# Kernel tuning notes

Measured on AMD Instinct MI355X. Metric: run time of the kernel, lower is better.

The kernel has to match this reference:

```python
import jax, jax.numpy as jnp
import numpy as np
import math

D = 1024
H = 16
DH = D // H
FF = 4096
B, S = 2, 2048


def _layernorm(x, g, b, eps=1e-5):
    mu = jnp.mean(x, axis=-1, keepdims=True)
    var = jnp.var(x, axis=-1, keepdims=True)
    return (x - mu) * jax.lax.rsqrt(var + eps) * g + b


def _gelu_tanh(x):
    # 0.5*x*(1+tanh(sqrt(2/pi)*(x+0.044715*x^3)))
    c = math.sqrt(2.0 / math.pi)
    return 0.5 * x * (1.0 + jnp.tanh(c * (x + 0.044715 * x ** 3)))


def setup_inputs() -> dict:
    key = jax.random.key(0)
    ks = jax.random.split(key, 8)
    s = 0.02
    return {
        "x": jax.random.normal(ks[0], (B, S, D), dtype=jnp.float32),
        "ln1_g": jnp.ones((D,), jnp.float32),
        "ln1_b": jnp.zeros((D,), jnp.float32),
        "Wqkv": jax.random.normal(ks[1], (D, 3 * D), jnp.float32) * s,
        "bqkv": jnp.zeros((3 * D,), jnp.float32),
        "Wo": jax.random.normal(ks[2], (D, D), jnp.float32) * s,
        "bo": jnp.zeros((D,), jnp.float32),
        "ln2_g": jnp.ones((D,), jnp.float32),
        "ln2_b": jnp.zeros((D,), jnp.float32),
        "W1": jax.random.normal(ks[3], (D, FF), jnp.float32) * s,
        "b1": jnp.zeros((FF,), jnp.float32),
        "W2": jax.random.normal(ks[4], (FF, D), jnp.float32) * s,
        "b2": jnp.zeros((D,), jnp.float32),
    }


def reference(x, ln1_g, ln1_b, Wqkv, bqkv, Wo, bo, ln2_g, ln2_b, W1, b1, W2, b2):
    b, s, d = x.shape
    h = _layernorm(x, ln1_g, ln1_b)
    qkv = h @ Wqkv + bqkv                       # [B,S,3D]
    q, k, v = jnp.split(qkv, 3, axis=-1)
    q = q.reshape(b, s, H, DH).transpose(0, 2, 1, 3)   # [B,H,S,Dh]
    k = k.reshape(b, s, H, DH).transpose(0, 2, 1, 3)
    v = v.reshape(b, s, H, DH).transpose(0, 2, 1, 3)
    scores = jnp.einsum("bhqd,bhkd->bhqk", q, k) / math.sqrt(DH)
    probs = jax.nn.softmax(scores, axis=-1)
    attn = jnp.einsum("bhqk,bhkd->bhqd", probs, v)     # [B,H,S,Dh]
    attn = attn.transpose(0, 2, 1, 3).reshape(b, s, d)
    attn = attn @ Wo + bo
    x = x + attn
    m = _layernorm(x, ln2_g, ln2_b)
    m = _gelu_tanh(m @ W1 + b1) @ W2 + b2
    return x + m
```

## Files before the change

### kernel.cpp

```cpp
#include <hip/hip_runtime.h>
#include <hip/hip_bf16.h>
#include <cstdint>

#define D_ 1024
#define H_ 16
#define DH_ 64
#define FF_ 4096
#define B_ 2
#define S_ 2048
#define MR_ (B_ * S_)

typedef __bf16 bf16x8 __attribute__((ext_vector_type(8)));
typedef __bf16 bf16x4 __attribute__((ext_vector_type(4)));
typedef float f32x4 __attribute__((ext_vector_type(4)));
typedef float f32x16 __attribute__((ext_vector_type(16)));

__device__ __forceinline__ void g2lds16(const void* g, void* l) {
  __builtin_amdgcn_global_load_lds(
      (__attribute__((address_space(1))) void*)(uintptr_t)g,
      (__attribute__((address_space(3))) void*)(uint32_t)(uintptr_t)l,
      16, 0, 0);
}

__device__ __forceinline__ unsigned pkbf16(float lo, float hi) {
  unsigned r;
  asm("v_cvt_pk_bf16_f32 %0, %1, %2" : "=v"(r) : "v"(lo), "v"(hi));
  return r;
}

__device__ __forceinline__ float fexp2(float x) {
  return __builtin_amdgcn_exp2f(x);
}

__global__ __launch_bounds__(256) void transpose_all(
    const float* __restrict__ W0, __hip_bfloat16* __restrict__ T0,
    const float* __restrict__ W1p, __hip_bfloat16* __restrict__ T1,
    const float* __restrict__ W2p, __hip_bfloat16* __restrict__ T2,
    const float* __restrict__ W3p, __hip_bfloat16* __restrict__ T3) {
  __shared__ float t[32][33];
  int ti = blockIdx.x;
  const float* W;
  __hip_bfloat16* Wt;
  int K, N, loc;
  if (ti < 3072)      { W = W0;  Wt = T0; K = 1024; N = 3072; loc = ti; }
  else if (ti < 4096) { W = W1p; Wt = T1; K = 1024; N = 1024; loc = ti - 3072; }
  else if (ti < 8192) { W = W2p; Wt = T2; K = 1024; N = 4096; loc = ti - 4096; }
  else                { W = W3p; Wt = T3; K = 4096; N = 1024; loc = ti - 8192; }
  int ntn = N >> 5;
  int bx = (loc % ntn) * 32;
  int by = (loc / ntn) * 32;
  int tx = threadIdx.x & 31, ty = threadIdx.x >> 5;
#pragma unroll
  for (int i = 0; i < 4; ++i)
    t[ty + 8 * i][tx] = W[(size_t)(by + ty + 8 * i) * N + bx + tx];
  __syncthreads();
#pragma unroll
  for (int i = 0; i < 4; ++i)
    Wt[(size_t)(bx + ty + 8 * i) * K + by + tx] = __float2bfloat16(t[tx][ty + 8 * i]);
}

__global__ __launch_bounds__(256) void ln_kernel(
    const float* __restrict__ x, const float* __restrict__ g,
    const float* __restrict__ b, __hip_bfloat16* __restrict__ out) {
  int row = blockIdx.x;
  const float4* xr = (const float4*)(x + (size_t)row * D_);
  float4 v = xr[threadIdx.x];
  float s = v.x + v.y + v.z + v.w;
  float ss = v.x * v.x + v.y * v.y + v.z * v.z + v.w * v.w;
#pragma unroll
  for (int m = 1; m < 64; m <<= 1) {
    s += __shfl_xor(s, m);
    ss += __shfl_xor(ss, m);
  }
  __shared__ float rs[4], rss[4];
  int wave = threadIdx.x >> 6, lane = threadIdx.x & 63;
  if (lane == 0) { rs[wave] = s; rss[wave] = ss; }
  __syncthreads();
  s = rs[0] + rs[1] + rs[2] + rs[3];
  ss = rss[0] + rss[1] + rss[2] + rss[3];
  float mean = s * (1.0f / D_);
  float var = ss * (1.0f / D_) - mean * mean;
  float inv = rsqrtf(var + 1e-5f);
  int c = threadIdx.x * 4;
  float4 gv = ((const float4*)g)[threadIdx.x];
  float4 bv = ((const float4*)b)[threadIdx.x];
  __hip_bfloat16* o = out + (size_t)row * D_ + c;
  o[0] = __float2bfloat16((v.x - mean) * inv * gv.x + bv.x);
  o[1] = __float2bfloat16((v.y - mean) * inv * gv.y + bv.y);
  o[2] = __float2bfloat16((v.z - mean) * inv * gv.z + bv.z);
  o[3] = __float2bfloat16((v.w - mean) * inv * gv.w + bv.w);
}

template <int EPI>
__global__ __launch_bounds__(256) void gemm4(
    const __hip_bfloat16* __restrict__ A, const __hip_bfloat16* __restrict__ Bt,
    const float* __restrict__ bias, const float* __restrict__ resid,
    void* __restrict__ outp, __hip_bfloat16* __restrict__ vt, int M, int N, int K) {
  constexpr int BM = 128, BN = 128, MF = 4, NF = 4;
  __shared__ alignas(16) __hip_bfloat16 sA[2][BM * 64];
  __shared__ alignas(16) __hip_bfloat16 sB[2][BN * 64];
  const int tid = threadIdx.x;
  const int lane = tid & 63, wave = tid >> 6;
  const int l15 = lane & 15, l4 = lane >> 4;
  const int wr = wave >> 1, wc = wave & 1;
  const int csw = (l15 & 7) << 3;

  const int gx = gridDim.x;
  int nwg = gx * gridDim.y;
  int flat = blockIdx.y * gx + blockIdx.x;
  int cpx = nwg >> 3;
  int swz = (flat & 7) * cpx + (flat >> 3);
  const int m0 = (swz / gx) * BM, n0 = (swz % gx) * BN;

  f32x4 z = {0.f, 0.f, 0.f, 0.f};
  f32x4 acc[MF][NF];
#pragma unroll
  for (int i = 0; i < MF; ++i)
#pragma unroll
    for (int j = 0; j < NF; ++j) acc[i][j] = z;

  auto stage = [&](int bu, int kt) {
#pragma unroll
    for (int it = 0; it < 4; ++it) {
      int idx = it * 256 + tid;
      int r = idx >> 3, c = (idx & 7) * 8;
      int cs = c ^ ((r & 7) << 3);
      g2lds16(A + (size_t)(m0 + r) * K + kt + cs, (void*)(&sA[bu][idx * 8]));
      g2lds16(Bt + (size_t)(n0 + r) * K + kt + cs, (void*)(&sB[bu][idx * 8]));
    }
  };

  const int nk = K / 64;
  stage(0, 0);
  asm volatile("s_waitcnt vmcnt(0)" ::: "memory");
  __builtin_amdgcn_s_barrier();

  for (int j = 0; j < nk; ++j) {
    const int cur = j & 1;
    if (j + 1 < nk) stage(cur ^ 1, (j + 1) * 64);

    __builtin_amdgcn_s_setprio(1);
#pragma unroll
    for (int kk = 0; kk < 2; ++kk) {
      int col = (kk * 32 + l4 * 8) ^ csw;
      bf16x8 bfr[NF];
#pragma unroll
      for (int nf = 0; nf < NF; ++nf)
        bfr[nf] = *(const bf16x8*)(&sB[cur][(wc * 64 + nf * 16 + l15) * 64 + col]);
#pragma unroll
      for (int mf = 0; mf < MF; ++mf) {
        bf16x8 af = *(const bf16x8*)(&sA[cur][(wr * 64 + mf * 16 + l15) * 64 + col]);
#pragma unroll
        for (int nf = 0; nf < NF; ++nf)
          acc[mf][nf] =
              __builtin_amdgcn_mfma_f32_16x16x32_bf16(af, bfr[nf], acc[mf][nf], 0, 0, 0);
      }
    }
    __builtin_amdgcn_s_setprio(0);

    asm volatile("s_waitcnt lgkmcnt(0)" ::: "memory");
    __builtin_amdgcn_sched_barrier(0);
    asm volatile("s_waitcnt vmcnt(0)" ::: "memory");
    __builtin_amdgcn_s_barrier();
    asm volatile("" ::: "memory");
  }

#pragma unroll
  for (int mf = 0; mf < MF; ++mf) {
#pragma unroll
    for (int nf = 0; nf < NF; ++nf) {
      int col = n0 + wc * 64 + nf * 16 + l15;
      float bv = bias[col];
      if (EPI == 3 && col >= 2 * D_) {
        int d = col - 2 * D_;
        int srow0 = m0 + wr * 64 + mf * 16 + l4 * 4;
        int bb = srow0 >> 11, s0 = srow0 & (S_ - 1);
        bf16x4 ov;
#pragma unroll
        for (int j = 0; j < 4; ++j) ov[j] = (__bf16)(acc[mf][nf][j] + bv);
        *(bf16x4*)(vt + ((size_t)(bb * H_ + (d >> 6)) * DH_ + (d & 63)) * S_ + s0) = ov;
      } else {
#pragma unroll
        for (int j = 0; j < 4; ++j) {
          int row = m0 + wr * 64 + mf * 16 + l4 * 4 + j;
          size_t o = (size_t)row * N + col;
          float v = acc[mf][nf][j] + bv;
          if (EPI == 0 || EPI == 3) {
            ((__hip_bfloat16*)outp)[o] = __float2bfloat16(v);
          } else if (EPI == 1) {
            ((float*)outp)[o] = v + resid[o];
          } else {
            float a = 0.7978845608028654f * (v + 0.044715f * v * v * v);
            a = fminf(fmaxf(a, -15.f), 15.f);
            float e = __expf(2.f * a);
            float th = (e - 1.f) / (e + 1.f);
            ((__hip_bfloat16*)outp)[o] = __float2bfloat16(0.5f * v * (1.f + th));
          }
        }
      }
    }
  }
}

template <int EPI>
__global__ __launch_bounds__(256) void gemm64r3(
    const __hip_bfloat16* __restrict__ A, const __hip_bfloat16* __restrict__ Bt,
    const float* __restrict__ bias, const float* __restrict__ resid,
    void* __restrict__ outp, int M, int N, int K) {
  constexpr int BM = 128, BN = 64, MF = 4, NF = 2;
  __shared__ alignas(16) __hip_bfloat16 sA[3][BM * 64];
  __shared__ alignas(16) __hip_bfloat16 sB[3][BN * 64];
  const int tid = threadIdx.x;
  const int lane = tid & 63, wave = tid >> 6;
  const int l15 = lane & 15, l4 = lane >> 4;
  const int wr = wave >> 1, wc = wave & 1;
  const int csw = (l15 & 7) << 3;

  const int gx = gridDim.x;
  int nwg = gx * gridDim.y;
  int flat = blockIdx.y * gx + blockIdx.x;
  int cpx = nwg >> 3;
  int swz = (flat & 7) * cpx + (flat >> 3);
  const int m0 = (swz / gx) * BM, n0 = (swz % gx) * BN;

  f32x4 z = {0.f, 0.f, 0.f, 0.f};
  f32x4 acc[MF][NF];
#pragma unroll
  for (int i = 0; i < MF; ++i)
#pragma unroll
    for (int j = 0; j < NF; ++j) acc[i][j] = z;

  auto stage = [&](int bu, int kt) {
#pragma unroll
    for (int it = 0; it < 4; ++it) {
      int idx = it * 256 + tid;
      int r = idx >> 3, c = (idx & 7) * 8;
      int cs = c ^ ((r & 7) << 3);
      g2lds16(A + (size_t)(m0 + r) * K + kt + cs, (void*)(&sA[bu][idx * 8]));
    }
#pragma unroll
    for (int it = 0; it < 2; ++it) {
      int idx = it * 256 + tid;
      int r = idx >> 3, c = (idx & 7) * 8;
      int cs = c ^ ((r & 7) << 3);
      g2lds16(Bt + (size_t)(n0 + r) * K + kt + cs, (void*)(&sB[bu][idx * 8]));
    }
  };

  const int nk = K / 64;
  stage(0, 0);
  stage(1, 64);
  asm volatile("s_waitcnt vmcnt(6)" ::: "memory");
  __builtin_amdgcn_s_barrier();

  int bu = 0, bu2 = 2;
  for (int j = 0; j < nk; ++j) {
    const bool pf = (j + 2) < nk;
    if (pf) stage(bu2, (j + 2) * 64);

    __builtin_amdgcn_s_setprio(1);
#pragma unroll
    for (int kk = 0; kk < 2; ++kk) {
      int col = (kk * 32 + l4 * 8) ^ csw;
      bf16x8 bfr[NF];
#pragma unroll
      for (int nf = 0; nf < NF; ++nf)
        bfr[nf] = *(const bf16x8*)(&sB[bu][(wc * 32 + nf * 16 + l15) * 64 + col]);
#pragma unroll
      for (int mf = 0; mf < MF; ++mf) {
        bf16x8 af = *(const bf16x8*)(&sA[bu][(wr * 64 + mf * 16 + l15) * 64 + col]);
#pragma unroll
        for (int nf = 0; nf < NF; ++nf)
          acc[mf][nf] =
              __builtin_amdgcn_mfma_f32_16x16x32_bf16(af, bfr[nf], acc[mf][nf], 0, 0, 0);
      }
    }
    __builtin_amdgcn_s_setprio(0);

    asm volatile("s_waitcnt lgkmcnt(0)" ::: "memory");
    __builtin_amdgcn_sched_barrier(0);
    if (pf)
      asm volatile("s_waitcnt vmcnt(6)" ::: "memory");
    else
      asm volatile("s_waitcnt vmcnt(0)" ::: "memory");
    __builtin_amdgcn_s_barrier();
    asm volatile("" ::: "memory");
    bu = (bu == 2) ? 0 : bu + 1;
    bu2 = (bu2 == 2) ? 0 : bu2 + 1;
  }

#pragma unroll
  for (int mf = 0; mf < MF; ++mf) {
#pragma unroll
    for (int nf = 0; nf < NF; ++nf) {
      int col = n0 + wc * 32 + nf * 16 + l15;
      float bv = bias[col];
#pragma unroll
      for (int j = 0; j < 4; ++j) {
        int row = m0 + wr * 64 + mf * 16 + l4 * 4 + j;
        size_t o = (size_t)row * N + col;
        float v = acc[mf][nf][j] + bv;
        if (EPI == 0) {
          ((__hip_bfloat16*)outp)[o] = __float2bfloat16(v);
        } else if (EPI == 1) {
          ((float*)outp)[o] = v + resid[o];
        } else {
          float a = 0.7978845608028654f * (v + 0.044715f * v * v * v);
          a = fminf(fmaxf(a, -15.f), 15.f);
          float e = __expf(2.f * a);
          float th = (e - 1.f) / (e + 1.f);
          ((__hip_bfloat16*)outp)[o] = __float2bfloat16(0.5f * v * (1.f + th));
        }
      }
    }
  }
}

template <int EPI>
__global__ __launch_bounds__(512, 1) void gemm256(
    const __hip_bfloat16* __restrict__ A, const __hip_bfloat16* __restrict__ Bt,
    const float* __restrict__ bias, const float* __restrict__ resid,
    void* __restrict__ outp, int M, int N, int K) {
  constexpr int BM = 256, BN = 256, MF = 8, NF = 4, WN = 4;
  __shared__ alignas(16) __hip_bfloat16 sA[2][BM * 64];
  __shared__ alignas(16) __hip_bfloat16 sB[2][BN * 64];
  const int tid = threadIdx.x;
  const int lane = tid & 63, wave = tid >> 6;
  const int l15 = lane & 15, l4 = lane >> 4;
  const int wr = wave / WN, wc = wave % WN;
  const int csw = (l15 & 7) << 3;

  const int gx = gridDim.x;
  int nwg = gx * gridDim.y;
  int flat = blockIdx.y * gx + blockIdx.x;
  int cpx = nwg >> 3;
  int swz = (flat & 7) * cpx + (flat >> 3);
  const int m0 = (swz / gx) * BM, n0 = (swz % gx) * BN;

  f32x4 z = {0.f, 0.f, 0.f, 0.f};
  f32x4 acc[MF][NF];
#pragma unroll
  for (int i = 0; i < MF; ++i)
#pragma unroll
    for (int j = 0; j < NF; ++j) acc[i][j] = z;

  auto stage = [&](int bu, int kt) {
#pragma unroll
    for (int it = 0; it < 4; ++it) {
      int idx = it * 512 + tid;
      int r = idx >> 3, c = (idx & 7) * 8;
      int cs = c ^ ((r & 7) << 3);
      g2lds16(A + (size_t)(m0 + r) * K + kt + cs, (void*)(&sA[bu][idx * 8]));
      g2lds16(Bt + (size_t)(n0 + r) * K + kt + cs, (void*)(&sB[bu][idx * 8]));
    }
  };

  const int nk = K / 64;
  stage(0, 0);
  asm volatile("s_waitcnt vmcnt(0)" ::: "memory");
  __builtin_amdgcn_s_barrier();

  for (int j = 0; j < nk; ++j) {
    const int cur = j & 1;
    if (j + 1 < nk) stage(cur ^ 1, (j + 1) * 64);

    __builtin_amdgcn_s_setprio(1);
#pragma unroll
    for (int kk = 0; kk < 2; ++kk) {
      int col = (kk * 32 + l4 * 8) ^ csw;
      bf16x8 bfr[NF];
#pragma unroll
      for (int nf = 0; nf < NF; ++nf)
        bfr[nf] = *(const bf16x8*)(&sB[cur][(wc * 64 + nf * 16 + l15) * 64 + col]);
#pragma unroll
      for (int mf = 0; mf < MF; ++mf) {
        bf16x8 af = *(const bf16x8*)(&sA[cur][(wr * 128 + mf * 16 + l15) * 64 + col]);
#pragma unroll
        for (int nf = 0; nf < NF; ++nf)
          acc[mf][nf] =
              __builtin_amdgcn_mfma_f32_16x16x32_bf16(af, bfr[nf], acc[mf][nf], 0, 0, 0);
      }
    }
    __builtin_amdgcn_s_setprio(0);

    asm volatile("s_waitcnt lgkmcnt(0)" ::: "memory");
    __builtin_amdgcn_sched_barrier(0);
    asm volatile("s_waitcnt vmcnt(0)" ::: "memory");
    __builtin_amdgcn_s_barrier();
    asm volatile("" ::: "memory");
  }

#pragma unroll
  for (int mf = 0; mf < MF; ++mf) {
#pragma unroll
    for (int nf = 0; nf < NF; ++nf) {
      int col = n0 + wc * 64 + nf * 16 + l15;
      float bv = bias[col];
#pragma unroll
      for (int j = 0; j < 4; ++j) {
        int row = m0 + wr * 128 + mf * 16 + l4 * 4 + j;
        size_t o = (size_t)row * N + col;
        float v = acc[mf][nf][j] + bv;
        if (EPI == 0) {
          ((__hip_bfloat16*)outp)[o] = __float2bfloat16(v);
        } else if (EPI == 1) {
          ((float*)outp)[o] = v + resid[o];
        } else {
          float a = 0.7978845608028654f * (v + 0.044715f * v * v * v);
          a = fminf(fmaxf(a, -15.f), 15.f);
          float e = __expf(2.f * a);
          float th = (e - 1.f) / (e + 1.f);
          ((__hip_bfloat16*)outp)[o] = __float2bfloat16(0.5f * v * (1.f + th));
        }
      }
    }
  }
}

__global__ __launch_bounds__(256, 2) void attn_kernel(
    const __hip_bfloat16* __restrict__ qkv, const __hip_bfloat16* __restrict__ vT,
    __hip_bfloat16* __restrict__ out) {
  __shared__ alignas(16) __hip_bfloat16 sK[2][2][64 * 64];
  __shared__ alignas(16) __hip_bfloat16 sV[2][2][64 * 64];
  const int tid = threadIdx.x, lane = tid & 63, wave = tid >> 6;
  const int l31 = lane & 31, hi = lane >> 5;
  const int bh = blockIdx.x, b = bh >> 4, h = bh & 15;
  const int q0 = blockIdx.y * 256;
  const int rsw = (l31 & 7) << 3;
  const float k2 = 0.125f * 1.44269504f;

  bf16x8 qfA[4], qfB[4];
  {
    int qrA = q0 + wave * 64 + l31;
    const size_t qbA = ((size_t)(b * S_ + qrA)) * (3 * D_) + h * DH_;
    const size_t qbB = qbA + (size_t)32 * (3 * D_);
#pragma unroll
    for (int ks = 0; ks < 4; ++ks) {
      bf16x8 qa = *(const bf16x8*)(qkv + qbA + ks * 16 + hi * 8);
      bf16x8 qb = *(const bf16x8*)(qkv + qbB + ks * 16 + hi * 8);
#pragma unroll
      for (int i = 0; i < 8; ++i) {
        qa[i] = (__bf16)((float)qa[i] * k2);
        qb[i] = (__bf16)((float)qb[i] * k2);
      }
      qfA[ks] = qa;
      qfB[ks] = qb;
    }
  }

  bf16x8 onesb;
#pragma unroll
  for (int i = 0; i < 8; ++i) onesb[i] = (__bf16)1.0f;

  f32x16 Z16;
#pragma unroll
  for (int r = 0; r < 16; ++r) Z16[r] = 0.f;

  f32x16 accA0 = Z16, accA1 = Z16, accLA = Z16;
  f32x16 accB0 = Z16, accB1 = Z16, accLB = Z16;

  const __hip_bfloat16* kg = qkv + (size_t)b * S_ * (3 * D_) + D_ + h * DH_;
  const __hip_bfloat16* vg = vT + (size_t)bh * DH_ * S_;

  auto stage = [&](int bu, int kv0) {
#pragma unroll
    for (int st = 0; st < 2; ++st) {
#pragma unroll
      for (int it = 0; it < 2; ++it) {
        int idx = it * 256 + tid;
        int r = idx >> 3;
        int c = (idx & 7) * 8;
        int cs = c ^ ((r & 7) << 3);
        g2lds16(kg + (size_t)(kv0 + st * 64 + r) * (3 * D_) + cs,
                (void*)(&sK[bu][st][idx * 8]));
        g2lds16(vg + (size_t)r * S_ + kv0 + st * 64 + cs,
                (void*)(&sV[bu][st][idx * 8]));
      }
    }
  };

  stage(0, 0);
  const int NT = S_ / 128;

  for (int t = 0; t < NT; ++t) {
    const int cur = t & 1;
    __syncthreads();
    if (t + 1 < NT) stage(cur ^ 1, (t + 1) * 128);

#pragma unroll
    for (int st = 0; st < 2; ++st) {
      const __hip_bfloat16* sKc = sK[cur][st];
      const __hip_bfloat16* sVc = sV[cur][st];

      f32x16 sfA0, sfA1, sfB0, sfB1;
      __builtin_amdgcn_s_setprio(1);
      {
        int colsw = (hi * 8) ^ rsw;
        bf16x8 kf0 = *(const bf16x8*)(&sKc[l31 * 64 + colsw]);
        bf16x8 kf1 = *(const bf16x8*)(&sKc[(32 + l31) * 64 + colsw]);
        sfA0 = __builtin_amdgcn_mfma_f32_32x32x16_bf16(kf0, qfA[0], Z16, 0, 0, 0);
        sfA1 = __builtin_amdgcn_mfma_f32_32x32x16_bf16(kf1, qfA[0], Z16, 0, 0, 0);
        sfB0 = __builtin_amdgcn_mfma_f32_32x32x16_bf16(kf0, qfB[0], Z16, 0, 0, 0);
        sfB1 = __builtin_amdgcn_mfma_f32_32x32x16_bf16(kf1, qfB[0], Z16, 0, 0, 0);
      }
#pragma unroll
      for (int ks = 1; ks < 4; ++ks) {
        int colsw = (ks * 16 + hi * 8) ^ rsw;
        bf16x8 kf0 = *(const bf16x8*)(&sKc[l31 * 64 + colsw]);
        bf16x8 kf1 = *(const bf16x8*)(&sKc[(32 + l31) * 64 + colsw]);
        sfA0 = __builtin_amdgcn_mfma_f32_32x32x16_bf16(kf0, qfA[ks], sfA0, 0, 0, 0);
        sfA1 = __builtin_amdgcn_mfma_f32_32x32x16_bf16(kf1, qfA[ks], sfA1, 0, 0, 0);
        sfB0 = __builtin_amdgcn_mfma_f32_32x32x16_bf16(kf0, qfB[ks], sfB0, 0, 0, 0);
        sfB1 = __builtin_amdgcn_mfma_f32_32x32x16_bf16(kf1, qfB[ks], sfB1, 0, 0, 0);
      }
      __builtin_amdgcn_s_setprio(0);

      bf16x8 paA[4], paB[4];
#pragma unroll
      for (int g = 0; g < 2; ++g) {
        const f32x16& s0 = g ? sfB0 : sfA0;
        const f32x16& s1 = g ? sfB1 : sfA1;
        bf16x8* pa = g ? paB : paA;
#pragma unroll
        for (int kb = 0; kb < 2; ++kb) {
          const f32x16& s16 = kb ? s1 : s0;
#pragma unroll
          for (int ksb = 0; ksb < 2; ++ksb) {
            float p0 = fexp2(s16[8 * ksb + 0]);
            float p1 = fexp2(s16[8 * ksb + 1]);
            float p2 = fexp2(s16[8 * ksb + 2]);
            float p3 = fexp2(s16[8 * ksb + 3]);
            float p4 = fexp2(s16[8 * ksb + 4]);
            float p5 = fexp2(s16[8 * ksb + 5]);
            float p6 = fexp2(s16[8 * ksb + 6]);
            float p7 = fexp2(s16[8 * ksb + 7]);
            unsigned wa = pkbf16(p0, p1), wb = pkbf16(p2, p3);
            unsigned wc = pkbf16(p4, p5), wd = pkbf16(p6, p7);
            auto r1 = __builtin_amdgcn_permlane32_swap(wa, wc, false, false);
            auto r2 = __builtin_amdgcn_permlane32_swap(wb, wd, false, false);
            union { unsigned u[4]; bf16x8 v; } w;
            w.u[0] = r1[0]; w.u[1] = r2[0]; w.u[2] = r1[1]; w.u[3] = r2[1];
            pa[kb * 2 + ksb] = w.v;
          }
        }
      }

      __builtin_amdgcn_s_setprio(1);
#pragma unroll
      for (int ksg = 0; ksg < 4; ++ksg) {
        int colsw = (ksg * 16 + hi * 8) ^ rsw;
        bf16x8 vf0 = *(const bf16x8*)(&sVc[l31 * 64 + colsw]);
        bf16x8 vf1 = *(const bf16x8*)(&sVc[(32 + l31) * 64 + colsw]);
        accA0 = __builtin_amdgcn_mfma_f32_32x32x16_bf16(paA[ksg], vf0, accA0, 0, 0, 0);
        accA1 = __builtin_amdgcn_mfma_f32_32x32x16_bf16(paA[ksg], vf1, accA1, 0, 0, 0);
        accLA = __builtin_amdgcn_mfma_f32_32x32x16_bf16(paA[ksg], onesb, accLA, 0, 0, 0);
        accB0 = __builtin_amdgcn_mfma_f32_32x32x16_bf16(paB[ksg], vf0, accB0, 0, 0, 0);
        accB1 = __builtin_amdgcn_mfma_f32_32x32x16_bf16(paB[ksg], vf1, accB1, 0, 0, 0);
        accLB = __builtin_amdgcn_mfma_f32_32x32x16_bf16(paB[ksg], onesb, accLB, 0, 0, 0);
      }
      __builtin_amdgcn_s_setprio(0);
    }
  }

#pragma unroll
  for (int r = 0; r < 16; ++r) {
    int qrow = (r & 3) + 8 * (r >> 2) + 4 * hi;
    size_t obA = ((size_t)(b * S_ + q0 + wave * 64 + qrow)) * D_ + h * DH_ + l31;
    size_t obB = obA + (size_t)32 * D_;
    float irA = 1.0f / accLA[r];
    float irB = 1.0f / accLB[r];
    out[obA] = __float2bfloat16(accA0[r] * irA);
    out[obA + 32] = __float2bfloat16(accA1[r] * irA);
    out[obB] = __float2bfloat16(accB0[r] * irB);
    out[obB + 32] = __float2bfloat16(accB1[r] * irB);
  }
}

extern "C" void kernel_launch(void* const* d_in, const int* in_sizes, int n_in,
                              void* d_out, int out_size, void* d_ws, size_t ws_size,
                              hipStream_t stream) {
  const float* x = (const float*)d_in[0];
  const float* ln1_g = (const float*)d_in[1];
  const float* ln1_b = (const float*)d_in[2];
  const float* Wqkv = (const float*)d_in[3];
  const float* bqkv = (const float*)d_in[4];
  const float* Wo = (const float*)d_in[5];
  const float* bo = (const float*)d_in[6];
  const float* ln2_g = (const float*)d_in[7];
  const float* ln2_b = (const float*)d_in[8];
  const float* W1 = (const float*)d_in[9];
  const float* b1 = (const float*)d_in[10];
  const float* W2 = (const float*)d_in[11];
  const float* b2 = (const float*)d_in[12];
  float* out = (float*)d_out;

  char* ws = (char*)d_ws;
  size_t off = 0;
  auto alloc = [&](size_t bytes) {
    void* p = ws + off;
    off += (bytes + 255) & ~(size_t)255;
    return p;
  };
  __hip_bfloat16* WqkvT = (__hip_bfloat16*)alloc((size_t)3 * D_ * D_ * 2);
  __hip_bfloat16* WoT = (__hip_bfloat16*)alloc((size_t)D_ * D_ * 2);
  __hip_bfloat16* W1T = (__hip_bfloat16*)alloc((size_t)FF_ * D_ * 2);
  __hip_bfloat16* W2T = (__hip_bfloat16*)alloc((size_t)D_ * FF_ * 2);
  __hip_bfloat16* h = (__hip_bfloat16*)alloc((size_t)MR_ * D_ * 2);
  __hip_bfloat16* qkv = (__hip_bfloat16*)alloc((size_t)MR_ * FF_ * 2);
  __hip_bfloat16* ff = qkv;
  __hip_bfloat16* vT = (__hip_bfloat16*)alloc((size_t)B_ * H_ * DH_ * S_ * 2);
  __hip_bfloat16* attn_out = (__hip_bfloat16*)alloc((size_t)MR_ * D_ * 2);

  transpose_all<<<dim3(12288), 256, 0, stream>>>(Wqkv, WqkvT, Wo, WoT, W1, W1T, W2, W2T);
  ln_kernel<<<MR_, 256, 0, stream>>>(x, ln1_g, ln1_b, h);
  gemm4<3><<<dim3(3 * D_ / 128, MR_ / 128), 256, 0, stream>>>(
      h, WqkvT, bqkv, nullptr, qkv, vT, MR_, 3 * D_, D_);
  attn_kernel<<<dim3(B_ * H_, S_ / 256), 256, 0, stream>>>(qkv, vT, attn_out);
  gemm64r3<1><<<dim3(D_ / 64, MR_ / 128), 256, 0, stream>>>(
      attn_out, WoT, bo, x, out, MR_, D_, D_);
  ln_kernel<<<MR_, 256, 0, stream>>>(out, ln2_g, ln2_b, h);
  gemm256<2><<<dim3(FF_ / 256, MR_ / 256), 512, 0, stream>>>(
      h, W1T, b1, nullptr, ff, MR_, FF_, D_);
  gemm64r3<1><<<dim3(D_ / 64, MR_ / 128), 256, 0, stream>>>(
      ff, W2T, b2, out, out, MR_, D_, FF_);
}
```

Before: 200.9 us.

## Issue both QK^T sub-tiles before softmax/PV and relax attention occupancy to one block

The attention inner loop now computes the QK^T scores for both 64-key sub-tiles up front, then runs exp/pack and the PV MMAs for each. This lets the exponentials of one sub-tile overlap with MFMA work instead of strictly alternating. The extra live score registers (eight f32x16 accumulators) are allowed for by lowering launch_bounds min blocks per CU from 2 to 1, trading occupancy for more registers. The s_setprio hints were also dropped.

```diff
diff --git a/kernel.cpp b/kernel.cpp
--- a/kernel.cpp
+++ b/kernel.cpp
@@ -417,7 +417,7 @@
   }
 }
 
-__global__ __launch_bounds__(256, 2) void attn_kernel(
+__global__ __launch_bounds__(256, 1) void attn_kernel(
     const __hip_bfloat16* __restrict__ qkv, const __hip_bfloat16* __restrict__ vT,
     __hip_bfloat16* __restrict__ out) {
   __shared__ alignas(16) __hip_bfloat16 sK[2][2][64 * 64];
@@ -479,6 +479,74 @@
     }
   };
 
+  auto qk = [&](const __hip_bfloat16* sKc, f32x16& s0, f32x16& s1,
+                f32x16& s2, f32x16& s3) {
+    {
+      int colsw = (hi * 8) ^ rsw;
+      bf16x8 kf0 = *(const bf16x8*)(&sKc[l31 * 64 + colsw]);
+      bf16x8 kf1 = *(const bf16x8*)(&sKc[(32 + l31) * 64 + colsw]);
+      s0 = __builtin_amdgcn_mfma_f32_32x32x16_bf16(kf0, qfA[0], Z16, 0, 0, 0);
+      s1 = __builtin_amdgcn_mfma_f32_32x32x16_bf16(kf1, qfA[0], Z16, 0, 0, 0);
+      s2 = __builtin_amdgcn_mfma_f32_32x32x16_bf16(kf0, qfB[0], Z16, 0, 0, 0);
+      s3 = __builtin_amdgcn_mfma_f32_32x32x16_bf16(kf1, qfB[0], Z16, 0, 0, 0);
+    }
+#pragma unroll
+    for (int ks = 1; ks < 4; ++ks) {
+      int colsw = (ks * 16 + hi * 8) ^ rsw;
+      bf16x8 kf0 = *(const bf16x8*)(&sKc[l31 * 64 + colsw]);
+      bf16x8 kf1 = *(const bf16x8*)(&sKc[(32 + l31) * 64 + colsw]);
+      s0 = __builtin_amdgcn_mfma_f32_32x32x16_bf16(kf0, qfA[ks], s0, 0, 0, 0);
+      s1 = __builtin_amdgcn_mfma_f32_32x32x16_bf16(kf1, qfA[ks], s1, 0, 0, 0);
+      s2 = __builtin_amdgcn_mfma_f32_32x32x16_bf16(kf0, qfB[ks], s2, 0, 0, 0);
+      s3 = __builtin_amdgcn_mfma_f32_32x32x16_bf16(kf1, qfB[ks], s3, 0, 0, 0);
+    }
+  };
+
+  auto smpv = [&](const __hip_bfloat16* sVc, const f32x16& sA0, const f32x16& sA1,
+                  const f32x16& sB0, const f32x16& sB1) {
+    bf16x8 paA[4], paB[4];
+#pragma unroll
+    for (int g = 0; g < 2; ++g) {
+      const f32x16& s0 = g ? sB0 : sA0;
+      const f32x16& s1 = g ? sB1 : sA1;
+      bf16x8* pa = g ? paB : paA;
+#pragma unroll
+      for (int kb = 0; kb < 2; ++kb) {
+        const f32x16& s16 = kb ? s1 : s0;
+#pragma unroll
+        for (int ksb = 0; ksb < 2; ++ksb) {
+          float p0 = fexp2(s16[8 * ksb + 0]);
+          float p1 = fexp2(s16[8 * ksb + 1]);
+          float p2 = fexp2(s16[8 * ksb + 2]);
+          float p3 = fexp2(s16[8 * ksb + 3]);
+          float p4 = fexp2(s16[8 * ksb + 4]);
+          float p5 = fexp2(s16[8 * ksb + 5]);
+          float p6 = fexp2(s16[8 * ksb + 6]);
+          float p7 = fexp2(s16[8 * ksb + 7]);
+          unsigned wa = pkbf16(p0, p1), wb = pkbf16(p2, p3);
+          unsigned wc = pkbf16(p4, p5), wd = pkbf16(p6, p7);
+          auto r1 = __builtin_amdgcn_permlane32_swap(wa, wc, false, false);
+          auto r2 = __builtin_amdgcn_permlane32_swap(wb, wd, false, false);
+          union { unsigned u[4]; bf16x8 v; } w;
+          w.u[0] = r1[0]; w.u[1] = r2[0]; w.u[2] = r1[1]; w.u[3] = r2[1];
+          pa[kb * 2 + ksb] = w.v;
+        }
+      }
+    }
+#pragma unroll
+    for (int ksg = 0; ksg < 4; ++ksg) {
+      int colsw = (ksg * 16 + hi * 8) ^ rsw;
+      bf16x8 vf0 = *(const bf16x8*)(&sVc[l31 * 64 + colsw]);
+      bf16x8 vf1 = *(const bf16x8*)(&sVc[(32 + l31) * 64 + colsw]);
+      accA0 = __builtin_amdgcn_mfma_f32_32x32x16_bf16(paA[ksg], vf0, accA0, 0, 0, 0);
+      accA1 = __builtin_amdgcn_mfma_f32_32x32x16_bf16(paA[ksg], vf1, accA1, 0, 0, 0);
+      accLA = __builtin_amdgcn_mfma_f32_32x32x16_bf16(paA[ksg], onesb, accLA, 0, 0, 0);
+      accB0 = __builtin_amdgcn_mfma_f32_32x32x16_bf16(paB[ksg], vf0, accB0, 0, 0, 0);
+      accB1 = __builtin_amdgcn_mfma_f32_32x32x16_bf16(paB[ksg], vf1, accB1, 0, 0, 0);
+      accLB = __builtin_amdgcn_mfma_f32_32x32x16_bf16(paB[ksg], onesb, accLB, 0, 0, 0);
+    }
+  };
+
   stage(0, 0);
   const int NT = S_ / 128;
 
@@ -487,79 +555,12 @@
     __syncthreads();
     if (t + 1 < NT) stage(cur ^ 1, (t + 1) * 128);
 
-#pragma unroll
-    for (int st = 0; st < 2; ++st) {
-      const __hip_bfloat16* sKc = sK[cur][st];
-      const __hip_bfloat16* sVc = sV[cur][st];
-
-      f32x16 sfA0, sfA1, sfB0, sfB1;
-      __builtin_amdgcn_s_setprio(1);
-      {
-        int colsw = (hi * 8) ^ rsw;
-        bf16x8 kf0 = *(const bf16x8*)(&sKc[l31 * 64 + colsw]);
-        bf16x8 kf1 = *(const bf16x8*)(&sKc[(32 + l31) * 64 + colsw]);
-        sfA0 = __builtin_amdgcn_mfma_f32_32x32x16_bf16(kf0, qfA[0], Z16, 0, 0, 0);
-        sfA1 = __builtin_amdgcn_mfma_f32_32x32x16_bf16(kf1, qfA[0], Z16, 0, 0, 0);
-        sfB0 = __builtin_amdgcn_mfma_f32_32x32x16_bf16(kf0, qfB[0], Z16, 0, 0, 0);
-        sfB1 = __builtin_amdgcn_mfma_f32_32x32x16_bf16(kf1, qfB[0], Z16, 0, 0, 0);
-      }
-#pragma unroll
-      for (int ks = 1; ks < 4; ++ks) {
-        int colsw = (ks * 16 + hi * 8) ^ rsw;
-        bf16x8 kf0 = *(const bf16x8*)(&sKc[l31 * 64 + colsw]);
-        bf16x8 kf1 = *(const bf16x8*)(&sKc[(32 + l31) * 64 + colsw]);
-        sfA0 = __builtin_amdgcn_mfma_f32_32x32x16_bf16(kf0, qfA[ks], sfA0, 0, 0, 0);
-        sfA1 = __builtin_amdgcn_mfma_f32_32x32x16_bf16(kf1, qfA[ks], sfA1, 0, 0, 0);
-        sfB0 = __builtin_amdgcn_mfma_f32_32x32x16_bf16(kf0, qfB[ks], sfB0, 0, 0, 0);
-        sfB1 = __builtin_amdgcn_mfma_f32_32x32x16_bf16(kf1, qfB[ks], sfB1, 0, 0, 0);
-      }
-      __builtin_amdgcn_s_setprio(0);
-
-      bf16x8 paA[4], paB[4];
-#pragma unroll
-      for (int g = 0; g < 2; ++g) {
-        const f32x16& s0 = g ? sfB0 : sfA0;
-        const f32x16& s1 = g ? sfB1 : sfA1;
-        bf16x8* pa = g ? paB : paA;
-#pragma unroll
-        for (int kb = 0; kb < 2; ++kb) {
-          const f32x16& s16 = kb ? s1 : s0;
-#pragma unroll
-          for (int ksb = 0; ksb < 2; ++ksb) {
-            float p0 = fexp2(s16[8 * ksb + 0]);
-            float p1 = fexp2(s16[8 * ksb + 1]);
-            float p2 = fexp2(s16[8 * ksb + 2]);
-            float p3 = fexp2(s16[8 * ksb + 3]);
-            float p4 = fexp2(s16[8 * ksb + 4]);
-            float p5 = fexp2(s16[8 * ksb + 5]);
-            float p6 = fexp2(s16[8 * ksb + 6]);
-            float p7 = fexp2(s16[8 * ksb + 7]);
-            unsigned wa = pkbf16(p0, p1), wb = pkbf16(p2, p3);
-            unsigned wc = pkbf16(p4, p5), wd = pkbf16(p6, p7);
-            auto r1 = __builtin_amdgcn_permlane32_swap(wa, wc, false, false);
-            auto r2 = __builtin_amdgcn_permlane32_swap(wb, wd, false, false);
-            union { unsigned u[4]; bf16x8 v; } w;
-            w.u[0] = r1[0]; w.u[1] = r2[0]; w.u[2] = r1[1]; w.u[3] = r2[1];
-            pa[kb * 2 + ksb] = w.v;
-          }
-        }
-      }
-
-      __builtin_amdgcn_s_setprio(1);
-#pragma unroll
-      for (int ksg = 0; ksg < 4; ++ksg) {
-        int colsw = (ksg * 16 + hi * 8) ^ rsw;
-        bf16x8 vf0 = *(const bf16x8*)(&sVc[l31 * 64 + colsw]);
-        bf16x8 vf1 = *(const bf16x8*)(&sVc[(32 + l31) * 64 + colsw]);
-        accA0 = __builtin_amdgcn_mfma_f32_32x32x16_bf16(paA[ksg], vf0, accA0, 0, 0, 0);
-        accA1 = __builtin_amdgcn_mfma_f32_32x32x16_bf16(paA[ksg], vf1, accA1, 0, 0, 0);
-        accLA = __builtin_amdgcn_mfma_f32_32x32x16_bf16(paA[ksg], onesb, accLA, 0, 0, 0);
-        accB0 = __builtin_amdgcn_mfma_f32_32x32x16_bf16(paB[ksg], vf0, accB0, 0, 0, 0);
-        accB1 = __builtin_amdgcn_mfma_f32_32x32x16_bf16(paB[ksg], vf1, accB1, 0, 0, 0);
-        accLB = __builtin_amdgcn_mfma_f32_32x32x16_bf16(paB[ksg], onesb, accLB, 0, 0, 0);
-      }
-      __builtin_amdgcn_s_setprio(0);
-    }
+    f32x16 s0A0, s0A1, s0B0, s0B1;
+    f32x16 s1A0, s1A1, s1B0, s1B1;
+    qk(sK[cur][0], s0A0, s0A1, s0B0, s0B1);
+    qk(sK[cur][1], s1A0, s1A1, s1B0, s1B1);
+    smpv(sV[cur][0], s0A0, s0A1, s0B0, s0B1);
+    smpv(sV[cur][1], s1A0, s1A1, s1B0, s1B1);
   }
 
 #pragma unroll
```

Result: no change. 202.7 us (+0.9%).
